# Optimization experiments

Hardware: AMD Instinct MI355X
Metric: run time of the kernel (lower is better)

Reference implementation:

```python
import jax, jax.numpy as jnp
import numpy as np

B, S, D, H = 2, 2048, 1024, 16
HD = D // H


def setup_inputs() -> dict:
    key = jax.random.key(0)
    ks = jax.random.split(key, 9)
    std = 0.02
    return {
        "x": jax.random.normal(ks[0], (B, S, D), dtype=jnp.float32),
        "wq": jax.random.normal(ks[1], (D, D), dtype=jnp.float32) * std,
        "bq": jnp.zeros((D,), dtype=jnp.float32),
        "wk": jax.random.normal(ks[2], (D, D), dtype=jnp.float32) * std,
        "bk": jnp.zeros((D,), dtype=jnp.float32),
        "wv": jax.random.normal(ks[3], (D, D), dtype=jnp.float32) * std,
        "bv": jnp.zeros((D,), dtype=jnp.float32),
        "wo": jax.random.normal(ks[4], (D, D), dtype=jnp.float32) * std,
        "bo": jnp.zeros((D,), dtype=jnp.float32),
    }


def reference(x, wq, bq, wk, bk, wv, bv, wo, bo):
    bsz, seq_len, d_model = x.shape
    # projections: torch Linear computes x @ W.T + b with W of shape (out, in)
    q = (x @ wq.T + bq).reshape(bsz, seq_len, H, HD).transpose(0, 2, 1, 3)  # bhsd
    k = (x @ wk.T + bk).reshape(bsz, seq_len, H, HD).transpose(0, 2, 1, 3)
    v = (x @ wv.T + bv).reshape(bsz, seq_len, H, HD).transpose(0, 2, 1, 3)
    scale = HD ** -0.5
    scores = jnp.einsum("bhqd,bhkd->bhqk", q, k) * scale  # [B,H,S,S]
    causal = jnp.tril(jnp.ones((seq_len, seq_len), dtype=bool))
    scores = jnp.where(causal[None, None], scores, -jnp.inf)
    attn = jax.nn.softmax(scores, axis=-1)
    ctx = jnp.einsum("bhqk,bhkd->bhqd", attn, v)
    ctx = ctx.transpose(0, 2, 1, 3).reshape(bsz, seq_len, d_model)
    return ctx @ wo.T + bo
```

## Files before the change

kernel.cpp:

```cpp
#include <hip/hip_runtime.h>
#include <hip/hip_bf16.h>

#define B_  2
#define S_  2048
#define D_  1024
#define H_  16
#define HD_ 64
#define M_  (B_ * S_)

typedef __bf16 bf16;
typedef __bf16 bf16x4 __attribute__((ext_vector_type(4)));
typedef __bf16 bf16x8 __attribute__((ext_vector_type(8)));
typedef float  f32x4  __attribute__((ext_vector_type(4)));
typedef unsigned int uint;

__device__ __forceinline__ bf16x8 ld8g(const bf16* p) { return *(const bf16x8*)p; }

#define GLL(g, l) __builtin_amdgcn_global_load_lds( \
    (const __attribute__((address_space(1))) void*)(g), \
    (__attribute__((address_space(3))) void*)(l), 16, 0, 0)

#define SWZ(row, byteoff) (((row) * 128) + ((byteoff) ^ (((row) & 7) << 4)))

__global__ __launch_bounds__(256) void convert_kernel(
    const float* __restrict__ x,  const float* __restrict__ wq,
    const float* __restrict__ wk, const float* __restrict__ wv,
    const float* __restrict__ wo,
    bf16* __restrict__ xb,  bf16* __restrict__ wqb, bf16* __restrict__ wkb,
    bf16* __restrict__ wvb, bf16* __restrict__ wob)
{
    const int seg = blockIdx.y;
    const float* src;
    bf16* dst;
    if (seg < 4)      { src = x  + (long)seg * 1048576; dst = xb  + (long)seg * 1048576; }
    else if (seg == 4){ src = wq; dst = wqb; }
    else if (seg == 5){ src = wk; dst = wkb; }
    else if (seg == 6){ src = wv; dst = wvb; }
    else              { src = wo; dst = wob; }
    const long i = ((long)blockIdx.x * 256 + threadIdx.x) * 8;
    float4 a = *(const float4*)(src + i);
    float4 b = *(const float4*)(src + i + 4);
    bf16x8 r;
    r[0] = (bf16)a.x; r[1] = (bf16)a.y; r[2] = (bf16)a.z; r[3] = (bf16)a.w;
    r[4] = (bf16)b.x; r[5] = (bf16)b.y; r[6] = (bf16)b.z; r[7] = (bf16)b.w;
    *(bf16x8*)(dst + i) = r;
}

__device__ __forceinline__ void gemm_acc_bk32(
    const bf16* __restrict__ A, const bf16* __restrict__ Bt,
    f32x4 (&acc)[4][4])
{
    __shared__ bf16 As[128 * 32];
    __shared__ bf16 Bs[128 * 32];

    const int tid  = threadIdx.x;
    const int wave = tid >> 6;
    const int lane = tid & 63;
    const int quad = lane >> 4;
    const int l15  = lane & 15;
    const int wr   = (wave >> 1) * 64;
    const int wc   = (wave & 1) * 64;
    const int m0   = blockIdx.y * 128;
    const int n0   = blockIdx.x * 128;

    const int sr = wave * 16 + (lane >> 2);
    const int sc = (lane & 3) * 8;
    const bf16* Ag = A  + (long)(m0 + sr) * D_ + sc;
    const bf16* Bg = Bt + (long)(n0 + sr) * D_ + sc;
    bf16* lA = As + wave * 512;
    bf16* lB = Bs + wave * 512;

    for (int k0 = 0; k0 < D_; k0 += 32) {
        __syncthreads();
        GLL(Ag + k0,             lA);
        GLL(Ag + 64 * D_ + k0,   lA + 64 * 32);
        GLL(Bg + k0,             lB);
        GLL(Bg + 64 * D_ + k0,   lB + 64 * 32);
        __syncthreads();

        bf16x8 af[4], bfr[4];
        for (int mi = 0; mi < 4; mi++)
            af[mi] = *(const bf16x8*)&As[(wr + mi * 16 + l15) * 32 + quad * 8];
        for (int ni = 0; ni < 4; ni++)
            bfr[ni] = *(const bf16x8*)&Bs[(wc + ni * 16 + l15) * 32 + quad * 8];

        for (int mi = 0; mi < 4; mi++)
            for (int ni = 0; ni < 4; ni++)
                acc[mi][ni] = __builtin_amdgcn_mfma_f32_16x16x32_bf16(
                    af[mi], bfr[ni], acc[mi][ni], 0, 0, 0);
    }
}

__global__ __launch_bounds__(256) void gemm_qkv(
    const bf16* __restrict__ xb,
    const bf16* __restrict__ wqb, const bf16* __restrict__ wkb, const bf16* __restrict__ wvb,
    const float* __restrict__ bq, const float* __restrict__ bk, const float* __restrict__ bv,
    bf16* __restrict__ qb, bf16* __restrict__ kb, bf16* __restrict__ vt)
{
    const bf16*  Bt   = (blockIdx.z == 0) ? wqb : (blockIdx.z == 1) ? wkb : wvb;
    const float* bias = (blockIdx.z == 0) ? bq  : (blockIdx.z == 1) ? bk  : bv;

    f32x4 acc[4][4] = {};
    gemm_acc_bk32(xb, Bt, acc);

    const int lane = threadIdx.x & 63;
    const int wave = threadIdx.x >> 6;
    const int quad = lane >> 4;
    const int l15  = lane & 15;
    const int wr   = (wave >> 1) * 64;
    const int wc   = (wave & 1) * 64;
    const int m0   = blockIdx.y * 128;
    const int n0   = blockIdx.x * 128;

    if (blockIdx.z < 2) {
        bf16* Cout = (blockIdx.z == 0) ? qb : kb;
        for (int ni = 0; ni < 4; ni++) {
            const int col = n0 + wc + ni * 16 + l15;
            const float bv = bias[col];
            for (int mi = 0; mi < 4; mi++) {
                const int rowb = m0 + wr + mi * 16 + quad * 4;
                for (int r = 0; r < 4; r++)
                    Cout[(long)(rowb + r) * D_ + col] = (bf16)(acc[mi][ni][r] + bv);
            }
        }
    } else {
        for (int ni = 0; ni < 4; ni++) {
            const int col = n0 + wc + ni * 16 + l15;
            const float bv = bias[col];
            const int h = col >> 6, hd = col & (HD_ - 1);
            for (int mi = 0; mi < 4; mi++) {
                const int rowb = m0 + wr + mi * 16 + quad * 4;
                const int b = rowb >> 11;
                const int s0 = rowb & (S_ - 1);
                bf16x4 v4;
                for (int r = 0; r < 4; r++) v4[r] = (bf16)(acc[mi][ni][r] + bv);
                *(bf16x4*)&vt[(((long)(b * H_ + h)) * HD_ + hd) * S_ + s0] = v4;
            }
        }
    }
}

__global__ __launch_bounds__(256) void gemm_out(
    const bf16* __restrict__ cb, const bf16* __restrict__ wob,
    const float* __restrict__ bo, float* __restrict__ out)
{
    __shared__ bf16 As[64 * 32];
    __shared__ bf16 Bs[128 * 32];

    const int tid  = threadIdx.x;
    const int wave = tid >> 6;
    const int lane = tid & 63;
    const int quad = lane >> 4;
    const int l15  = lane & 15;
    const int wr   = (wave >> 1) * 32;
    const int wc   = (wave & 1) * 64;
    const int m0   = blockIdx.y * 64;
    const int n0   = blockIdx.x * 128;

    const int sr = tid >> 2;
    const int scg = (tid & 3) * 8;
    const bf16* Ag = cb  + (long)(m0 + sr) * D_ + scg;
    const bf16* Bg = wob + (long)(n0 + sr) * D_ + scg;
    bf16* lA = As + wave * 512;
    bf16* lB = Bs + wave * 512;

    f32x4 acc[2][4] = {};
    for (int k0 = 0; k0 < D_; k0 += 32) {
        __syncthreads();
        GLL(Ag + k0,            lA);
        GLL(Bg + k0,            lB);
        GLL(Bg + 64 * D_ + k0,  lB + 64 * 32);
        __syncthreads();

        bf16x8 af[2], bfr[4];
        for (int mi = 0; mi < 2; mi++)
            af[mi] = *(const bf16x8*)&As[(wr + mi * 16 + l15) * 32 + quad * 8];
        for (int ni = 0; ni < 4; ni++)
            bfr[ni] = *(const bf16x8*)&Bs[(wc + ni * 16 + l15) * 32 + quad * 8];

        for (int mi = 0; mi < 2; mi++)
            for (int ni = 0; ni < 4; ni++)
                acc[mi][ni] = __builtin_amdgcn_mfma_f32_16x16x32_bf16(
                    af[mi], bfr[ni], acc[mi][ni], 0, 0, 0);
    }

    for (int ni = 0; ni < 4; ni++) {
        const int col = n0 + wc + ni * 16 + l15;
        const float bv = bo[col];
        for (int mi = 0; mi < 2; mi++) {
            const int rowb = m0 + wr + mi * 16 + quad * 4;
            for (int r = 0; r < 4; r++)
                out[(long)(rowb + r) * D_ + col] = acc[mi][ni][r] + bv;
        }
    }
}

__global__ __launch_bounds__(512, 4) void attn_kernel(
    const bf16* __restrict__ Q, const bf16* __restrict__ K,
    const bf16* __restrict__ vt, bf16* __restrict__ ctx)
{
    __shared__ bf16 Ks[2][64 * 64];
    __shared__ bf16 Vt[2][64 * 64];

    const int tid  = threadIdx.x;
    const int wave = tid >> 6;
    const int lane = tid & 63;
    const int quad = lane >> 4;
    const int l15  = lane & 15;
    const int bh   = blockIdx.y;
    const int qt   = (blockIdx.y < 16) ? blockIdx.x : (15 - (int)blockIdx.x);
    const int b    = bh >> 4, h = bh & 15;
    const long base = ((long)b * S_) * D_ + h * HD_;
    const bf16* Kg  = K + base;
    const bf16* Vth = vt + (long)bh * HD_ * S_;

    char* K0 = (char*)&Ks[0][0]; char* K1 = (char*)&Ks[1][0];
    char* V0 = (char*)&Vt[0][0]; char* V1 = (char*)&Vt[1][0];

    const int rho  = wave * 8 + (lane >> 3);
    const int chnk = lane & 7;
    const int scol = ((chnk ^ (rho & 7)) * 8);
    const int gK = (rho & 32) + ((rho >> 3) & 1) * 16 + ((rho >> 2) & 1) * 8
                 + ((rho >> 4) & 1) * 4 + (rho & 3);
    const bf16* KgL = Kg  + (long)gK  * D_ + scol;
    const bf16* VgL = Vth + (long)rho * S_ + scol;
    bf16* Kw0 = (bf16*)(K0 + wave * 1024);
    bf16* Vw0 = (bf16*)(V0 + wave * 1024);
    bf16* Kw1 = (bf16*)(K1 + wave * 1024);
    bf16* Vw1 = (bf16*)(V1 + wave * 1024);

    const int qw   = qt * 128 + wave * 16;
    const int qrow = qw + l15;
    const bf16* Qr = Q + base + (long)qrow * D_;
    bf16x8 qf0 = ld8g(&Qr[quad * 8]);
    bf16x8 qf1 = ld8g(&Qr[quad * 8 + 32]);

    float l_i = 0.f;
    f32x4 o_acc[4] = {};

    auto process_tile = [&](int kbase, int buf) {
        if (kbase > qw + 15) return;
        const char* Kb = buf ? K1 : K0;
        const char* Vb = buf ? V1 : V0;

        f32x4 sc[4];
        __builtin_amdgcn_s_setprio(1);
        #pragma unroll
        for (int kt = 0; kt < 4; kt++) {
            bf16x8 a0 = *(const bf16x8*)(Kb + SWZ(kt * 16 + l15, quad * 16));
            bf16x8 a1 = *(const bf16x8*)(Kb + SWZ(kt * 16 + l15, quad * 16 + 64));
            f32x4 z = {};
            z = __builtin_amdgcn_mfma_f32_16x16x32_bf16(a0, qf0, z, 0, 0, 0);
            z = __builtin_amdgcn_mfma_f32_16x16x32_bf16(a1, qf1, z, 0, 0, 0);
            sc[kt] = z;
        }
        __builtin_amdgcn_s_setprio(0);

        float sum = 0.f;
        if (kbase + 63 <= qw) {
            #pragma unroll
            for (int kt = 0; kt < 4; kt++)
                #pragma unroll
                for (int r = 0; r < 4; r++) {
                    const float p = __expf(sc[kt][r] * 0.125f);
                    sc[kt][r] = p;
                    sum += p;
                }
        } else {
            #pragma unroll
            for (int kt = 0; kt < 4; kt++)
                #pragma unroll
                for (int r = 0; r < 4; r++) {
                    const int kg = kbase + (kt >> 1) * 32 + quad * 8 + (kt & 1) * 4 + r;
                    const float p = (kg <= qrow) ? __expf(sc[kt][r] * 0.125f) : 0.f;
                    sc[kt][r] = p;
                    sum += p;
                }
        }
        sum += __shfl_xor(sum, 16, 64);
        sum += __shfl_xor(sum, 32, 64);
        l_i += sum;

        union { bf16 hh[8]; bf16x8 v; } pa0, pa1;
        #pragma unroll
        for (int r = 0; r < 4; r++) {
            pa0.hh[r]     = (bf16)sc[0][r];
            pa0.hh[r + 4] = (bf16)sc[1][r];
            pa1.hh[r]     = (bf16)sc[2][r];
            pa1.hh[r + 4] = (bf16)sc[3][r];
        }

        __builtin_amdgcn_s_setprio(1);
        #pragma unroll
        for (int ni = 0; ni < 4; ni++) {
            bf16x8 av0 = *(const bf16x8*)(Vb + SWZ(ni * 16 + l15, quad * 16));
            bf16x8 av1 = *(const bf16x8*)(Vb + SWZ(ni * 16 + l15, quad * 16 + 64));
            o_acc[ni] = __builtin_amdgcn_mfma_f32_16x16x32_bf16(av0, pa0.v, o_acc[ni], 0, 0, 0);
            o_acc[ni] = __builtin_amdgcn_mfma_f32_16x16x32_bf16(av1, pa1.v, o_acc[ni], 0, 0, 0);
        }
        __builtin_amdgcn_s_setprio(0);
    };

    GLL(KgL, Kw0);
    GLL(VgL, Vw0);
    __syncthreads();

    const int njt = 2 * qt + 2;
    for (int j = 0; j < njt; ++j) {
        const int cur = j & 1;
        if (j + 1 < njt) {
            GLL(KgL + (long)(j + 1) * 64 * D_, cur ? Kw0 : Kw1);
            GLL(VgL + (j + 1) * 64,            cur ? Vw0 : Vw1);
        }
        process_tile(j * 64, cur);
        __syncthreads();
    }

    char* epi = (char*)&Ks[0][0] + wave * 2048;
    const float inv = 1.f / l_i;
    #pragma unroll
    for (int ni = 0; ni < 4; ni++) {
        union { uint2 u; bf16 hh[4]; } pk;
        pk.hh[0] = (bf16)(o_acc[ni][0] * inv);
        pk.hh[1] = (bf16)(o_acc[ni][1] * inv);
        pk.hh[2] = (bf16)(o_acc[ni][2] * inv);
        pk.hh[3] = (bf16)(o_acc[ni][3] * inv);
        *(uint2*)(epi + SWZ(l15, ni * 32 + quad * 8)) = pk.u;
    }
    __asm__ volatile("s_waitcnt lgkmcnt(0)" ::: "memory");
    __builtin_amdgcn_sched_barrier(0);
    #pragma unroll
    for (int round = 0; round < 2; round++) {
        const int rowq = (lane >> 3) + round * 8;
        bf16x8 val = *(const bf16x8*)(epi + SWZ(rowq, (lane & 7) * 16));
        const int q_g = qt * 128 + wave * 16 + rowq;
        *(bf16x8*)&ctx[base + (long)q_g * D_ + (lane & 7) * 8] = val;
    }
}

extern "C" void kernel_launch(void* const* d_in, const int* in_sizes, int n_in,
                              void* d_out, int out_size, void* d_ws, size_t ws_size,
                              hipStream_t stream)
{
    const float* x  = (const float*)d_in[0];
    const float* wq = (const float*)d_in[1];
    const float* bq = (const float*)d_in[2];
    const float* wk = (const float*)d_in[3];
    const float* bk = (const float*)d_in[4];
    const float* wv = (const float*)d_in[5];
    const float* bv = (const float*)d_in[6];
    const float* wo = (const float*)d_in[7];
    const float* bo = (const float*)d_in[8];
    float* out = (float*)d_out;

    const long NX = (long)M_ * D_;
    const long NW = (long)D_ * D_;
    bf16* xb  = (bf16*)d_ws;
    bf16* wqb = xb  + NX;
    bf16* wkb = wqb + NW;
    bf16* wvb = wkb + NW;
    bf16* wob = wvb + NW;
    bf16* qb  = wob + NW;
    bf16* kb  = qb  + NX;
    bf16* vt  = kb  + NX;
    bf16* cb  = xb;

    dim3 blk(256, 1, 1);

    convert_kernel<<<dim3(512, 8), blk, 0, stream>>>(
        x, wq, wk, wv, wo, xb, wqb, wkb, wvb, wob);

    gemm_qkv<<<dim3(8, 32, 3), blk, 0, stream>>>(
        xb, wqb, wkb, wvb, bq, bk, bv, qb, kb, vt);

    attn_kernel<<<dim3(16, 32), dim3(512, 1, 1), 0, stream>>>(qb, kb, vt, cb);

    gemm_out<<<dim3(8, 64), blk, 0, stream>>>(cb, wob, bo, out);
}
```

Measured before the change: 177.8 us.

## Deepen attention K/V pipeline to four LDS stages with explicit vmcnt waits

Replaces the double-buffered K/V staging in the attention kernel with a four-slot ring buffer that keeps up to three tiles in flight. Each iteration waits with counted s_waitcnt vmcnt and a single barrier instead of a full __syncthreads after every tile. The aim is to hide global-to-LDS load latency better. LDS use doubles to 64KB per block, which may cut occupancy below the 4-blocks launch bound and reduce latency hiding across blocks.

```diff
diff --git a/kernel.cpp b/kernel.cpp
--- a/kernel.cpp
+++ b/kernel.cpp
@@ -199,8 +199,8 @@
     const bf16* __restrict__ Q, const bf16* __restrict__ K,
     const bf16* __restrict__ vt, bf16* __restrict__ ctx)
 {
-    __shared__ bf16 Ks[2][64 * 64];
-    __shared__ bf16 Vt[2][64 * 64];
+    __shared__ bf16 Ks[4][64 * 64];
+    __shared__ bf16 Vt[4][64 * 64];
 
     const int tid  = threadIdx.x;
     const int wave = tid >> 6;
@@ -214,8 +214,9 @@
     const bf16* Kg  = K + base;
     const bf16* Vth = vt + (long)bh * HD_ * S_;
 
-    char* K0 = (char*)&Ks[0][0]; char* K1 = (char*)&Ks[1][0];
-    char* V0 = (char*)&Vt[0][0]; char* V1 = (char*)&Vt[1][0];
+    char* KsB = (char*)&Ks[0][0];
+    char* VtB = (char*)&Vt[0][0];
+    const int woff = wave * 1024;
 
     const int rho  = wave * 8 + (lane >> 3);
     const int chnk = lane & 7;
@@ -224,10 +225,6 @@
                  + ((rho >> 4) & 1) * 4 + (rho & 3);
     const bf16* KgL = Kg  + (long)gK  * D_ + scol;
     const bf16* VgL = Vth + (long)rho * S_ + scol;
-    bf16* Kw0 = (bf16*)(K0 + wave * 1024);
-    bf16* Vw0 = (bf16*)(V0 + wave * 1024);
-    bf16* Kw1 = (bf16*)(K1 + wave * 1024);
-    bf16* Vw1 = (bf16*)(V1 + wave * 1024);
 
     const int qw   = qt * 128 + wave * 16;
     const int qrow = qw + l15;
@@ -240,8 +237,8 @@
 
     auto process_tile = [&](int kbase, int buf) {
         if (kbase > qw + 15) return;
-        const char* Kb = buf ? K1 : K0;
-        const char* Vb = buf ? V1 : V0;
+        const char* Kb = KsB + buf * 8192;
+        const char* Vb = VtB + buf * 8192;
 
         f32x4 sc[4];
         __builtin_amdgcn_s_setprio(1);
@@ -301,22 +298,34 @@
         __builtin_amdgcn_s_setprio(0);
     };
 
-    GLL(KgL, Kw0);
-    GLL(VgL, Vw0);
+    const int njt = 2 * qt + 2;
+
+    GLL(KgL,               (bf16*)(KsB + 0 * 8192 + woff));
+    GLL(VgL,               (bf16*)(VtB + 0 * 8192 + woff));
+    GLL(KgL + 64 * D_,     (bf16*)(KsB + 1 * 8192 + woff));
+    GLL(VgL + 64,          (bf16*)(VtB + 1 * 8192 + woff));
+    if (njt > 2) {
+        GLL(KgL + 2 * 64 * D_, (bf16*)(KsB + 2 * 8192 + woff));
+        GLL(VgL + 2 * 64,      (bf16*)(VtB + 2 * 8192 + woff));
+    }
+
+    for (int j = 0; j < njt; ++j) {
+        const int rem = njt - 1 - j;
+        if (rem >= 2)      asm volatile("s_waitcnt vmcnt(4)" ::: "memory");
+        else if (rem == 1) asm volatile("s_waitcnt vmcnt(2)" ::: "memory");
+        else               asm volatile("s_waitcnt vmcnt(0)" ::: "memory");
+        __builtin_amdgcn_s_barrier();
+        __builtin_amdgcn_sched_barrier(0);
+        if (j + 3 < njt) {
+            const int bi = (j + 3) & 3;
+            GLL(KgL + (long)(j + 3) * 64 * D_, (bf16*)(KsB + bi * 8192 + woff));
+            GLL(VgL + (j + 3) * 64,            (bf16*)(VtB + bi * 8192 + woff));
+        }
+        process_tile(j * 64, j & 3);
+    }
+
     __syncthreads();
-
-    const int njt = 2 * qt + 2;
-    for (int j = 0; j < njt; ++j) {
-        const int cur = j & 1;
-        if (j + 1 < njt) {
-            GLL(KgL + (long)(j + 1) * 64 * D_, cur ? Kw0 : Kw1);
-            GLL(VgL + (j + 1) * 64,            cur ? Vw0 : Vw1);
-        }
-        process_tile(j * 64, cur);
-        __syncthreads();
-    }
-
-    char* epi = (char*)&Ks[0][0] + wave * 2048;
+    char* epi = KsB + wave * 2048;
     const float inv = 1.f / l_i;
     #pragma unroll
     for (int ni = 0; ni < 4; ni++) {
```

Result: slower. 183.4 us (+3.1%).
